# Kernel optimization log

Measured on AMD Instinct MI355X. Metric: run time of the kernel, lower is better.

The kernel has to match this reference:

```python
import jax, jax.numpy as jnp
import numpy as np

N_LEVELS = 16
N_FEATS = 2
LOG2_T = 19
TABLE_SIZE = 1 << LOG2_T
BASE_RES = 16
FINEST_RES = 512
DIM = 3
N_POINTS = 2_000_000
PRIMES = jnp.array([1, 2654435761, 805459861], dtype=jnp.uint32)


def _hash_encode(x01, tables, resolutions):
    """Multi-resolution hash grid encoding with trilinear interpolation.
    x01: [N, D] in [0, 1]; tables: [L, T, F]; resolutions: [L] float.
    Returns [N, L*F]."""
    N, D = x01.shape
    T = tables.shape[1]
    # all 2^D corner offsets of the enclosing voxel, shape [2^D, D]
    offsets = jnp.array([[(i >> d) & 1 for d in range(D)] for i in range(1 << D)],
                        dtype=jnp.float32)

    def per_level(table, res):
        pos = x01 * res                      # [N, D]
        p0 = jnp.floor(pos)
        w = pos - p0                         # fractional part, [N, D]
        corners = p0[None, :, :] + offsets[:, None, :]      # [2^D, N, D]
        ci = corners.astype(jnp.uint32)
        hp = ci * PRIMES[None, None, :D]                    # uint32 wraps mod 2^32
        h = hp[..., 0]
        for d in range(1, D):
            h = h ^ hp[..., d]
        idx = (h & jnp.uint32(T - 1)).astype(jnp.int32)     # [2^D, N]
        feats = table[idx]                                  # gather, [2^D, N, F]
        # trilinear weights: prod_d (w_d if corner bit set else 1-w_d)
        wc = jnp.prod(jnp.where(offsets[:, None, :] > 0, w[None], 1.0 - w[None]),
                      axis=-1)                              # [2^D, N]
        return jnp.sum(wc[..., None] * feats, axis=0)       # [N, F]

    f = jax.vmap(per_level)(tables, resolutions)            # [L, N, F]
    return jnp.transpose(f, (1, 0, 2)).reshape(N, -1)       # [N, L*F]


def setup_inputs() -> dict:
    key = jax.random.key(0)
    ks = jax.random.split(key, 8)
    x = jax.random.uniform(ks[0], (N_POINTS, DIM), jnp.float32, -1.0, 1.0)
    tables = jax.random.uniform(ks[1], (N_LEVELS, TABLE_SIZE, N_FEATS),
                                jnp.float32, -1e-4, 1e-4)
    b = np.exp((np.log(FINEST_RES) - np.log(BASE_RES)) / (N_LEVELS - 1))
    resolutions = jnp.asarray(np.floor(BASE_RES * b ** np.arange(N_LEVELS)),
                              dtype=jnp.float32)
    in_dim = N_LEVELS * N_FEATS  # 32
    W1 = jax.random.normal(ks[2], (in_dim, 64), jnp.float32) * (1.0 / np.sqrt(in_dim))
    b1 = jnp.zeros((64,), jnp.float32)
    W2 = jax.random.normal(ks[3], (64, 64), jnp.float32) * (1.0 / 8.0)
    b2 = jnp.zeros((64,), jnp.float32)
    W3 = jax.random.normal(ks[4], (64, 1), jnp.float32) * (1.0 / 8.0)
    b3 = jnp.zeros((1,), jnp.float32)
    return {"x": x, "tables": tables, "resolutions": resolutions,
            "W1": W1, "b1": b1, "W2": W2, "b2": b2, "W3": W3, "b3": b3}


def reference(x, tables, resolutions, W1, b1, W2, b2, W3, b3):
    x01 = x / 2.0 + 0.5                       # map [-1,1] -> [0,1]
    a = _hash_encode(x01, tables, resolutions)  # [N, 32]
    h = jax.nn.relu(a @ W1 + b1)
    h = jax.nn.relu(h @ W2 + b2)
    return h @ W3 + b3                        # [N, 1]
```

## Files before the change

kernel.cpp:

```cpp
#include <hip/hip_runtime.h>
#include <hip/hip_bf16.h>
#include <stdint.h>

#define N_LEVELS   16
#define LOG2_T     19
#define TABLE_SIZE (1u << LOG2_T)
#define PRIME_Y    2654435761u
#define PRIME_Z    805459861u

#define NB        32768
#define SORT_B    256

typedef float v4f __attribute__((ext_vector_type(4)));
typedef _Float16 v8h __attribute__((ext_vector_type(8)));

__device__ __forceinline__ uint32_t part1by2(uint32_t v) {
    v &= 0x3FFu;
    v = (v | (v << 16)) & 0x030000FFu;
    v = (v | (v <<  8)) & 0x0300F00Fu;
    v = (v | (v <<  4)) & 0x030C30C3u;
    v = (v | (v <<  2)) & 0x09249249u;
    return v;
}
__device__ __forceinline__ uint32_t morton_key(float xr, float yr, float zr) {
    int vx = (int)((xr * 0.5f + 0.5f) * 32.0f);
    int vy = (int)((yr * 0.5f + 0.5f) * 32.0f);
    int vz = (int)((zr * 0.5f + 0.5f) * 32.0f);
    vx = vx < 0 ? 0 : (vx > 31 ? 31 : vx);
    vy = vy < 0 ? 0 : (vy > 31 ? 31 : vy);
    vz = vz < 0 ? 0 : (vz > 31 ? 31 : vz);
    return part1by2((uint32_t)vx) | (part1by2((uint32_t)vy) << 1)
         | (part1by2((uint32_t)vz) << 2);
}

__global__ __launch_bounds__(256)
void hist_kernel(const float* __restrict__ x, uint32_t* __restrict__ g_hist,
                 int n, int chunk)
{
    __shared__ uint32_t pack[NB / 2];
    const int b = blockIdx.x, t = threadIdx.x;
    for (int w = t; w < NB / 2; w += 256) pack[w] = 0;
    __syncthreads();
    const int beg = b * chunk;
    const int end = (beg + chunk < n) ? (beg + chunk) : n;
    for (int i = beg + t; i < end; i += 256) {
        const uint32_t key = morton_key(x[3*i], x[3*i+1], x[3*i+2]);
        atomicAdd(&pack[key >> 1], 1u << ((key & 1u) << 4));
    }
    __syncthreads();
    uint32_t* __restrict__ dst = g_hist + (size_t)b * NB;
    for (int w = t; w < NB / 2; w += 256) {
        const uint32_t p = pack[w];
        dst[2*w]     = p & 0xFFFFu;
        dst[2*w + 1] = p >> 16;
    }
}

__global__ __launch_bounds__(256)
void scan_cols_kernel(const uint32_t* __restrict__ g_hist,
                      uint32_t* __restrict__ g_part,
                      uint32_t* __restrict__ totals)
{
    const int key = blockIdx.x * 256 + threadIdx.x;
    uint32_t run = 0;
    #pragma unroll 8
    for (int b = 0; b < SORT_B; ++b) {
        const size_t idx = (size_t)b * NB + key;
        const uint32_t v = g_hist[idx];
        g_part[idx] = run;
        run += v;
    }
    totals[key] = run;
}

__global__ void scan_block_kernel(const uint32_t* __restrict__ counts,
                                  uint32_t* __restrict__ prefix,
                                  uint32_t* __restrict__ blocksum) {
    __shared__ uint32_t s[256];
    const int t = threadIdx.x;
    const int i = blockIdx.x * 256 + t;
    const uint32_t v = counts[i];
    s[t] = v; __syncthreads();
    #pragma unroll
    for (int d = 1; d < 256; d <<= 1) {
        const uint32_t u = (t >= d) ? s[t - d] : 0;
        __syncthreads();
        s[t] += u;
        __syncthreads();
    }
    prefix[i] = s[t] - v;
    if (t == 255) blocksum[blockIdx.x] = s[255];
}

__global__ void scan_top_kernel(const uint32_t* __restrict__ blocksum,
                                uint32_t* __restrict__ blockbase, int nb) {
    __shared__ uint32_t s[1024];
    const int t = threadIdx.x;
    const uint32_t v = (t < nb) ? blocksum[t] : 0;
    s[t] = v; __syncthreads();
    #pragma unroll
    for (int d = 1; d < 1024; d <<= 1) {
        const uint32_t u = (t >= d) ? s[t - d] : 0;
        __syncthreads();
        s[t] += u;
        __syncthreads();
    }
    if (t < nb) blockbase[t] = s[t] - v;
}

__global__ void addback_kernel(const uint32_t* __restrict__ prefix,
                               const uint32_t* __restrict__ blockbase,
                               uint32_t* __restrict__ base) {
    const int i = blockIdx.x * 256 + threadIdx.x;
    base[i] = prefix[i] + blockbase[i >> 8];
}

__global__ __launch_bounds__(256)
void scatter_kernel(const float* __restrict__ x,
                    const uint32_t* __restrict__ base,
                    const uint32_t* __restrict__ g_part,
                    float* __restrict__ xs,
                    int* __restrict__ rank_inv,
                    int n, int chunk)
{
    __shared__ uint32_t pack[NB / 2];
    const int b = blockIdx.x, t = threadIdx.x;
    for (int w = t; w < NB / 2; w += 256) pack[w] = 0;
    __syncthreads();
    const uint32_t* __restrict__ part = g_part + (size_t)b * NB;
    const int beg = b * chunk;
    const int end = (beg + chunk < n) ? (beg + chunk) : n;
    for (int i = beg + t; i < end; i += 256) {
        const float a = x[3*i], c = x[3*i+1], d = x[3*i+2];
        const uint32_t key = morton_key(a, c, d);
        const uint32_t sh = (key & 1u) << 4;
        uint32_t r = atomicAdd(&pack[key >> 1], 1u << sh);
        r = (r >> sh) & 0xFFFFu;
        const uint32_t pos = base[key] + part[key] + r;
        xs[pos]         = a;
        xs[n + pos]     = c;
        xs[2*n + pos]   = d;
        rank_inv[i]     = (int)pos;
    }
}

__global__ __launch_bounds__(256, 8)
void encode_kernel(const float* __restrict__ xs,
                   const float* __restrict__ tables,
                   const float* __restrict__ resolutions,
                   _Float16* __restrict__ a_ws,
                   int n)
{
    const int l = blockIdx.y;
    int p = blockIdx.x * blockDim.x + threadIdx.x;
    if (p >= n) p = n - 1;

    const float x0 = xs[p]       * 0.5f + 0.5f;
    const float x1 = xs[n + p]   * 0.5f + 0.5f;
    const float x2 = xs[2*n + p] * 0.5f + 0.5f;

    const float res = resolutions[l];
    const float px = x0 * res, py = x1 * res, pz = x2 * res;
    const float fx = floorf(px), fy = floorf(py), fz = floorf(pz);
    const float wx = px - fx, wy = py - fy, wz = pz - fz;
    const uint32_t cx = (uint32_t)fx;
    const uint32_t cy = (uint32_t)fy;
    const uint32_t cz = (uint32_t)fz;

    const uint32_t hy0 = cy * PRIME_Y, hy1 = hy0 + PRIME_Y;
    const uint32_t hz0 = cz * PRIME_Z, hz1 = hz0 + PRIME_Z;

    const float wx0 = 1.0f - wx, wy0 = 1.0f - wy, wz0 = 1.0f - wz;

    const float* __restrict__ tab = tables + (size_t)l * (size_t)TABLE_SIZE * 2u;

    const uint32_t hyz[4] = { hy0 ^ hz0, hy1 ^ hz0, hy0 ^ hz1, hy1 ^ hz1 };

    float2 cva[4], cvb[4];

    if ((cx & 1u) == 0u) {
        #pragma unroll
        for (int q = 0; q < 4; ++q) {
            const uint32_t idx_a = (cx ^ hyz[q]) & (TABLE_SIZE - 1u);
            const uint32_t base  = idx_a & ~1u;
            const float4 f4 = *(const float4*)(tab + 2u * base);
            const bool hi = (idx_a & 1u) != 0u;
            cva[q] = hi ? make_float2(f4.z, f4.w) : make_float2(f4.x, f4.y);
            cvb[q] = hi ? make_float2(f4.x, f4.y) : make_float2(f4.z, f4.w);
        }
    } else {
        const uint32_t hx0 = cx, hx1 = cx + 1u;
        #pragma unroll
        for (int q = 0; q < 4; ++q) {
            const uint32_t idx_a = (hx0 ^ hyz[q]) & (TABLE_SIZE - 1u);
            const uint32_t idx_b = (hx1 ^ hyz[q]) & (TABLE_SIZE - 1u);
            cva[q] = *(const float2*)(tab + 2u * idx_a);
            cvb[q] = *(const float2*)(tab + 2u * idx_b);
        }
    }

    float f0 = 0.0f, f1 = 0.0f;
    #pragma unroll
    for (int q = 0; q < 4; ++q) {
        const float yf = (q & 1) ? wy : wy0;
        const float zf = (q & 2) ? wz : wz0;
        const float wgt_a = (wx0 * yf) * zf;
        const float wgt_b = (wx  * yf) * zf;
        f0 = fmaf(wgt_a, cva[q].x, f0);
        f1 = fmaf(wgt_a, cva[q].y, f1);
        f0 = fmaf(wgt_b, cvb[q].x, f0);
        f1 = fmaf(wgt_b, cvb[q].y, f1);
    }

    a_ws[(size_t)(2 * l + 0) * n + p] = (_Float16)(f0 * 256.0f);
    a_ws[(size_t)(2 * l + 1) * n + p] = (_Float16)(f1 * 256.0f);
}

__global__ __launch_bounds__(256, 2)
void mlp_mfma_kernel(const _Float16* __restrict__ a_ws,
                     const float* __restrict__ W1,
                     const float* __restrict__ b1,
                     const float* __restrict__ W2,
                     const float* __restrict__ b2,
                     const float* __restrict__ W3,
                     const float* __restrict__ b3,
                     float* __restrict__ outs,
                     int n)
{
    __shared__ float lds[4 * 64 * 16];

    const int lane    = threadIdx.x & 63;
    const int wave_id = threadIdx.x >> 6;
    const int m       = lane & 15;
    const int q       = lane >> 4;
    float* __restrict__ myl = &lds[wave_id * 1024];

    const float b3s = b3[0];

    v8h a1[4];
    #pragma unroll
    for (int t = 0; t < 4; ++t)
        #pragma unroll
        for (int j = 0; j < 8; ++j)
            a1[t][j] = (_Float16)W1[(8 * q + j) * 64 + 16 * t + m];

    v8h a2[2][4];
    #pragma unroll
    for (int c = 0; c < 2; ++c)
        #pragma unroll
        for (int t = 0; t < 4; ++t)
            #pragma unroll
            for (int j = 0; j < 8; ++j)
                a2[c][t][j] = (_Float16)W2[(32 * c + 8 * q + j) * 64 + 16 * t + m];

    float bias1v[16], bias2v[16], w3v[16];
    #pragma unroll
    for (int t = 0; t < 4; ++t)
        #pragma unroll
        for (int r = 0; r < 4; ++r) {
            const int ch = 16 * t + 4 * q + r;
            bias1v[4 * t + r] = 256.0f * b1[ch];
            bias2v[4 * t + r] = 256.0f * b2[ch];
            w3v[4 * t + r]    = W3[ch];
        }

    const int nt = (n + 15) >> 4;
    const int stride = gridDim.x * 4;
    const int gw = blockIdx.x * 4 + wave_id;
    if (gw >= nt) return;

    v8h bh;
    {
        const int p0 = gw * 16;
        const int pr = (p0 + m < n) ? (p0 + m) : (n - 1);
        #pragma unroll
        for (int j = 0; j < 8; ++j)
            bh[j] = a_ws[(size_t)(8 * q + j) * n + pr];
    }

    for (int tile = gw; tile < nt; tile += stride) {
        const int p0 = tile * 16;

        v8h bhn = bh;
        const int nx = tile + stride;
        if (nx < nt) {
            const int p0n = nx * 16;
            const int prn = (p0n + m < n) ? (p0n + m) : (n - 1);
            #pragma unroll
            for (int j = 0; j < 8; ++j)
                bhn[j] = a_ws[(size_t)(8 * q + j) * n + prn];
        }

        v4f acc1[4];
        #pragma unroll
        for (int t = 0; t < 4; ++t) {
            #pragma unroll
            for (int r = 0; r < 4; ++r) acc1[t][r] = bias1v[4 * t + r];
            acc1[t] = __builtin_amdgcn_mfma_f32_16x16x32_f16(a1[t], bh, acc1[t], 0, 0, 0);
        }

        #pragma unroll
        for (int t = 0; t < 4; ++t)
            #pragma unroll
            for (int r = 0; r < 4; ++r)
                myl[(16 * t + 4 * q + r) * 16 + m] = fmaxf(acc1[t][r], 0.0f);
        __threadfence_block();

        v8h b2h[2];
        #pragma unroll
        for (int c = 0; c < 2; ++c)
            #pragma unroll
            for (int j = 0; j < 8; ++j)
                b2h[c][j] = (_Float16)myl[(32 * c + 8 * q + j) * 16 + m];

        v4f acc2[4];
        #pragma unroll
        for (int t = 0; t < 4; ++t) {
            #pragma unroll
            for (int r = 0; r < 4; ++r) acc2[t][r] = bias2v[4 * t + r];
            acc2[t] = __builtin_amdgcn_mfma_f32_16x16x32_f16(a2[0][t], b2h[0], acc2[t], 0, 0, 0);
            acc2[t] = __builtin_amdgcn_mfma_f32_16x16x32_f16(a2[1][t], b2h[1], acc2[t], 0, 0, 0);
        }

        float partial = 0.0f;
        #pragma unroll
        for (int t = 0; t < 4; ++t)
            #pragma unroll
            for (int r = 0; r < 4; ++r)
                partial = fmaf(fmaxf(acc2[t][r], 0.0f), w3v[4 * t + r], partial);

        partial += __shfl_xor(partial, 16);
        partial += __shfl_xor(partial, 32);

        if (q == 0 && p0 + m < n)
            outs[p0 + m] = partial * (1.0f / 256.0f) + b3s;

        bh = bhn;
    }
}

__global__ void unscatter_kernel(const float* __restrict__ outs,
                                 const int* __restrict__ rank_inv,
                                 float* __restrict__ out, int n) {
    const int i = blockIdx.x * blockDim.x + threadIdx.x;
    if (i < n) out[i] = outs[rank_inv[i]];
}

__global__ __launch_bounds__(256, 4)
void hashgrid_mlp_fused(const float* __restrict__ x,
                        const float* __restrict__ tables,
                        const float* __restrict__ resolutions,
                        const float* __restrict__ W1,
                        const float* __restrict__ b1,
                        const float* __restrict__ W2,
                        const float* __restrict__ b2,
                        const float* __restrict__ W3,
                        const float* __restrict__ b3,
                        float* __restrict__ out,
                        int n)
{
    const int i  = blockIdx.x * blockDim.x + threadIdx.x;
    const int ip = (i < n) ? i : (n - 1);

    const float x0 = x[3 * ip + 0] * 0.5f + 0.5f;
    const float x1 = x[3 * ip + 1] * 0.5f + 0.5f;
    const float x2 = x[3 * ip + 2] * 0.5f + 0.5f;

    float h1[64];
    #pragma unroll
    for (int j = 0; j < 64; ++j) h1[j] = b1[j];

    #pragma unroll
    for (int l = 0; l < N_LEVELS; ++l) {
        const float res = resolutions[l];
        const float px = x0 * res, py = x1 * res, pz = x2 * res;
        const float fx = floorf(px), fy = floorf(py), fz = floorf(pz);
        const float wx = px - fx, wy = py - fy, wz = pz - fz;
        const uint32_t cx = (uint32_t)fx;
        const uint32_t cy = (uint32_t)fy;
        const uint32_t cz = (uint32_t)fz;
        const uint32_t hx0 = cx,           hx1 = cx + 1u;
        const uint32_t hy0 = cy * PRIME_Y, hy1 = hy0 + PRIME_Y;
        const uint32_t hz0 = cz * PRIME_Z, hz1 = hz0 + PRIME_Z;
        const float wx0 = 1.0f - wx, wy0 = 1.0f - wy, wz0 = 1.0f - wz;
        const float* __restrict__ tab = tables + (size_t)l * (size_t)TABLE_SIZE * 2u;

        float f0 = 0.0f, f1 = 0.0f;
        #pragma unroll
        for (int c = 0; c < 8; ++c) {
            const uint32_t h = ((c & 1) ? hx1 : hx0) ^
                               ((c & 2) ? hy1 : hy0) ^
                               ((c & 4) ? hz1 : hz0);
            const uint32_t idx = h & (TABLE_SIZE - 1u);
            const float2 fv = *(const float2*)(tab + 2u * idx);
            const float wgt = ((c & 1) ? wx : wx0) *
                              ((c & 2) ? wy : wy0) *
                              ((c & 4) ? wz : wz0);
            f0 = fmaf(wgt, fv.x, f0);
            f1 = fmaf(wgt, fv.y, f1);
        }
        const float* __restrict__ w1a = W1 + (2 * l + 0) * 64;
        const float* __restrict__ w1b = W1 + (2 * l + 1) * 64;
        #pragma unroll
        for (int j = 0; j < 64; ++j)
            h1[j] = fmaf(f1, w1b[j], fmaf(f0, w1a[j], h1[j]));
    }

    #pragma unroll
    for (int j = 0; j < 64; ++j) h1[j] = fmaxf(h1[j], 0.0f);

    float accum = b3[0];
    #pragma unroll
    for (int half = 0; half < 2; ++half) {
        float h2[32];
        #pragma unroll
        for (int j = 0; j < 32; ++j) h2[j] = b2[half * 32 + j];
        #pragma unroll
        for (int k = 0; k < 64; ++k) {
            const float hk = h1[k];
            const float* __restrict__ w2row = W2 + k * 64 + half * 32;
            #pragma unroll
            for (int j = 0; j < 32; ++j)
                h2[j] = fmaf(hk, w2row[j], h2[j]);
        }
        #pragma unroll
        for (int j = 0; j < 32; ++j)
            accum = fmaf(fmaxf(h2[j], 0.0f), W3[half * 32 + j], accum);
    }
    out[ip] = accum;
}

extern "C" void kernel_launch(void* const* d_in, const int* in_sizes, int n_in,
                              void* d_out, int out_size, void* d_ws, size_t ws_size,
                              hipStream_t stream) {
    const float* x           = (const float*)d_in[0];
    const float* tables      = (const float*)d_in[1];
    const float* resolutions = (const float*)d_in[2];
    const float* W1          = (const float*)d_in[3];
    const float* b1          = (const float*)d_in[4];
    const float* W2          = (const float*)d_in[5];
    const float* b2          = (const float*)d_in[6];
    const float* W3          = (const float*)d_in[7];
    const float* b3          = (const float*)d_in[8];
    float* out               = (float*)d_out;

    const int n = out_size;
    const int block = 256;
    const int grid_pts = (n + block - 1) / block;
    const int chunk = (n + SORT_B - 1) / SORT_B;

    size_t off = 0;
    #define CARVE(bytes) (off = (off + 255) & ~(size_t)255, off += (bytes), off - (bytes))
    const size_t aws_off   = CARVE((size_t)32 * n * sizeof(_Float16));
    const size_t xs_off    = CARVE((size_t)3 * n * sizeof(float));
    const size_t rank_off  = CARVE((size_t)n * sizeof(int));
    const size_t outs_off  = CARVE((size_t)n * sizeof(float));
    const size_t tot_off   = CARVE((size_t)NB * sizeof(uint32_t));
    const size_t pref_off  = CARVE((size_t)NB * sizeof(uint32_t));
    const size_t base_off  = CARVE((size_t)NB * sizeof(uint32_t));
    const size_t bsum_off  = CARVE(1024 * sizeof(uint32_t));
    const size_t bbase_off = CARVE(1024 * sizeof(uint32_t));
    const size_t total_ws  = off;
    #undef CARVE

    if (ws_size >= total_ws) {
        char* ws = (char*)d_ws;
        _Float16* a_ws   = (_Float16*)(ws + aws_off);
        uint32_t* g_hist = (uint32_t*)(ws + aws_off);
        uint32_t* g_part = (uint32_t*)(ws + aws_off + (size_t)SORT_B * NB * 4);
        float*    xs     = (float*)(ws + xs_off);
        int*      rank   = (int*)(ws + rank_off);
        float*    outs   = (float*)(ws + outs_off);
        uint32_t* totals = (uint32_t*)(ws + tot_off);
        uint32_t* pref   = (uint32_t*)(ws + pref_off);
        uint32_t* base   = (uint32_t*)(ws + base_off);
        uint32_t* bsum   = (uint32_t*)(ws + bsum_off);
        uint32_t* bbase  = (uint32_t*)(ws + bbase_off);

        hist_kernel<<<SORT_B, block, 0, stream>>>(x, g_hist, n, chunk);
        scan_cols_kernel<<<NB / 256, block, 0, stream>>>(g_hist, g_part, totals);
        scan_block_kernel<<<NB / 256, block, 0, stream>>>(totals, pref, bsum);
        scan_top_kernel<<<1, 1024, 0, stream>>>(bsum, bbase, NB / 256);
        addback_kernel<<<NB / 256, block, 0, stream>>>(pref, bbase, base);
        scatter_kernel<<<SORT_B, block, 0, stream>>>(x, base, g_part, xs, rank, n, chunk);

        dim3 grid_enc(grid_pts, N_LEVELS);
        encode_kernel<<<grid_enc, block, 0, stream>>>(xs, tables, resolutions, a_ws, n);
        mlp_mfma_kernel<<<1024, block, 0, stream>>>(a_ws, W1, b1, W2, b2, W3, b3, outs, n);
        unscatter_kernel<<<grid_pts, block, 0, stream>>>(outs, rank, out, n);
    } else {
        hashgrid_mlp_fused<<<grid_pts, block, 0, stream>>>(
            x, tables, resolutions, W1, b1, W2, b2, W3, b3, out, n);
    }
}
```

Measured before the change: 671.0 us.

## Pack sorted coords as float4, pair features per level, fold unscatter into MLP

The scatter kernel now writes sorted coordinates as one float4 per point and records the inverse permutation (sorted position to original index). The encoder reads a single float4 and writes both features of a level as one packed 32-bit word with a nontemporal store. The MLP kernel reads those packed words with nontemporal loads and writes results straight to the original order through perm. This removes the separate unscatter kernel and its intermediate buffer, and cuts the number of memory transactions. The cost is an extra padding float per point and scattered final writes.

```diff
diff --git a/kernel.cpp b/kernel.cpp
--- a/kernel.cpp
+++ b/kernel.cpp
@@ -119,8 +119,8 @@
 void scatter_kernel(const float* __restrict__ x,
                     const uint32_t* __restrict__ base,
                     const uint32_t* __restrict__ g_part,
-                    float* __restrict__ xs,
-                    int* __restrict__ rank_inv,
+                    float4* __restrict__ xs4,
+                    int* __restrict__ perm,
                     int n, int chunk)
 {
     __shared__ uint32_t pack[NB / 2];
@@ -137,27 +137,26 @@
         uint32_t r = atomicAdd(&pack[key >> 1], 1u << sh);
         r = (r >> sh) & 0xFFFFu;
         const uint32_t pos = base[key] + part[key] + r;
-        xs[pos]         = a;
-        xs[n + pos]     = c;
-        xs[2*n + pos]   = d;
-        rank_inv[i]     = (int)pos;
+        xs4[pos]  = make_float4(a, c, d, 0.0f);
+        perm[pos] = i;
     }
 }
 
 __global__ __launch_bounds__(256, 8)
-void encode_kernel(const float* __restrict__ xs,
+void encode_kernel(const float4* __restrict__ xs4,
                    const float* __restrict__ tables,
                    const float* __restrict__ resolutions,
-                   _Float16* __restrict__ a_ws,
+                   uint32_t* __restrict__ a_ws2,
                    int n)
 {
     const int l = blockIdx.y;
     int p = blockIdx.x * blockDim.x + threadIdx.x;
     if (p >= n) p = n - 1;
 
-    const float x0 = xs[p]       * 0.5f + 0.5f;
-    const float x1 = xs[n + p]   * 0.5f + 0.5f;
-    const float x2 = xs[2*n + p] * 0.5f + 0.5f;
+    const float4 xv = xs4[p];
+    const float x0 = xv.x * 0.5f + 0.5f;
+    const float x1 = xv.y * 0.5f + 0.5f;
+    const float x2 = xv.z * 0.5f + 0.5f;
 
     const float res = resolutions[l];
     const float px = x0 * res, py = x1 * res, pz = x2 * res;
@@ -212,19 +211,22 @@
         f1 = fmaf(wgt_b, cvb[q].y, f1);
     }
 
-    a_ws[(size_t)(2 * l + 0) * n + p] = (_Float16)(f0 * 256.0f);
-    a_ws[(size_t)(2 * l + 1) * n + p] = (_Float16)(f1 * 256.0f);
+    union { _Float16 h[2]; uint32_t u; } pk;
+    pk.h[0] = (_Float16)(f0 * 256.0f);
+    pk.h[1] = (_Float16)(f1 * 256.0f);
+    __builtin_nontemporal_store(pk.u, a_ws2 + (size_t)l * n + p);
 }
 
 __global__ __launch_bounds__(256, 2)
-void mlp_mfma_kernel(const _Float16* __restrict__ a_ws,
+void mlp_mfma_kernel(const uint32_t* __restrict__ a_ws2,
                      const float* __restrict__ W1,
                      const float* __restrict__ b1,
                      const float* __restrict__ W2,
                      const float* __restrict__ b2,
                      const float* __restrict__ W3,
                      const float* __restrict__ b3,
-                     float* __restrict__ outs,
+                     const int* __restrict__ perm,
+                     float* __restrict__ out,
                      int n)
 {
     __shared__ float lds[4 * 64 * 16];
@@ -269,13 +271,18 @@
     const int gw = blockIdx.x * 4 + wave_id;
     if (gw >= nt) return;
 
+    union BF { uint32_t w[4]; v8h h; };
+
     v8h bh;
     {
         const int p0 = gw * 16;
         const int pr = (p0 + m < n) ? (p0 + m) : (n - 1);
-        #pragma unroll
-        for (int j = 0; j < 8; ++j)
-            bh[j] = a_ws[(size_t)(8 * q + j) * n + pr];
+        BF ub;
+        #pragma unroll
+        for (int lv = 0; lv < 4; ++lv)
+            ub.w[lv] = __builtin_nontemporal_load(
+                a_ws2 + (size_t)(4 * q + lv) * n + pr);
+        bh = ub.h;
     }
 
     for (int tile = gw; tile < nt; tile += stride) {
@@ -286,9 +293,12 @@
         if (nx < nt) {
             const int p0n = nx * 16;
             const int prn = (p0n + m < n) ? (p0n + m) : (n - 1);
-            #pragma unroll
-            for (int j = 0; j < 8; ++j)
-                bhn[j] = a_ws[(size_t)(8 * q + j) * n + prn];
+            BF ub;
+            #pragma unroll
+            for (int lv = 0; lv < 4; ++lv)
+                ub.w[lv] = __builtin_nontemporal_load(
+                    a_ws2 + (size_t)(4 * q + lv) * n + prn);
+            bhn = ub.h;
         }
 
         v4f acc1[4];
@@ -333,17 +343,10 @@
         partial += __shfl_xor(partial, 32);
 
         if (q == 0 && p0 + m < n)
-            outs[p0 + m] = partial * (1.0f / 256.0f) + b3s;
+            out[perm[p0 + m]] = partial * (1.0f / 256.0f) + b3s;
 
         bh = bhn;
     }
-}
-
-__global__ void unscatter_kernel(const float* __restrict__ outs,
-                                 const int* __restrict__ rank_inv,
-                                 float* __restrict__ out, int n) {
-    const int i = blockIdx.x * blockDim.x + threadIdx.x;
-    if (i < n) out[i] = outs[rank_inv[i]];
 }
 
 __global__ __launch_bounds__(256, 4)
@@ -451,10 +454,9 @@
 
     size_t off = 0;
     #define CARVE(bytes) (off = (off + 255) & ~(size_t)255, off += (bytes), off - (bytes))
-    const size_t aws_off   = CARVE((size_t)32 * n * sizeof(_Float16));
-    const size_t xs_off    = CARVE((size_t)3 * n * sizeof(float));
-    const size_t rank_off  = CARVE((size_t)n * sizeof(int));
-    const size_t outs_off  = CARVE((size_t)n * sizeof(float));
+    const size_t aws_off   = CARVE((size_t)16 * n * sizeof(uint32_t));
+    const size_t xs_off    = CARVE((size_t)n * sizeof(float4));
+    const size_t perm_off  = CARVE((size_t)n * sizeof(int));
     const size_t tot_off   = CARVE((size_t)NB * sizeof(uint32_t));
     const size_t pref_off  = CARVE((size_t)NB * sizeof(uint32_t));
     const size_t base_off  = CARVE((size_t)NB * sizeof(uint32_t));
@@ -465,12 +467,11 @@
 
     if (ws_size >= total_ws) {
         char* ws = (char*)d_ws;
-        _Float16* a_ws   = (_Float16*)(ws + aws_off);
+        uint32_t* a_ws2  = (uint32_t*)(ws + aws_off);
         uint32_t* g_hist = (uint32_t*)(ws + aws_off);
         uint32_t* g_part = (uint32_t*)(ws + aws_off + (size_t)SORT_B * NB * 4);
-        float*    xs     = (float*)(ws + xs_off);
-        int*      rank   = (int*)(ws + rank_off);
-        float*    outs   = (float*)(ws + outs_off);
+        float4*   xs4    = (float4*)(ws + xs_off);
+        int*      perm   = (int*)(ws + perm_off);
         uint32_t* totals = (uint32_t*)(ws + tot_off);
         uint32_t* pref   = (uint32_t*)(ws + pref_off);
         uint32_t* base   = (uint32_t*)(ws + base_off);
@@ -482,12 +483,12 @@
         scan_block_kernel<<<NB / 256, block, 0, stream>>>(totals, pref, bsum);
         scan_top_kernel<<<1, 1024, 0, stream>>>(bsum, bbase, NB / 256);
         addback_kernel<<<NB / 256, block, 0, stream>>>(pref, bbase, base);
-        scatter_kernel<<<SORT_B, block, 0, stream>>>(x, base, g_part, xs, rank, n, chunk);
+        scatter_kernel<<<SORT_B, block, 0, stream>>>(x, base, g_part, xs4, perm, n, chunk);
 
         dim3 grid_enc(grid_pts, N_LEVELS);
-        encode_kernel<<<grid_enc, block, 0, stream>>>(xs, tables, resolutions, a_ws, n);
-        mlp_mfma_kernel<<<1024, block, 0, stream>>>(a_ws, W1, b1, W2, b2, W3, b3, outs, n);
-        unscatter_kernel<<<grid_pts, block, 0, stream>>>(outs, rank, out, n);
+        encode_kernel<<<grid_enc, block, 0, stream>>>(xs4, tables, resolutions, a_ws2, n);
+        mlp_mfma_kernel<<<1024, block, 0, stream>>>(a_ws2, W1, b1, W2, b2, W3, b3,
+                                                    perm, out, n);
     } else {
         hashgrid_mlp_fused<<<grid_pts, block, 0, stream>>>(
             x, tables, resolutions, W1, b1, W2, b2, W3, b3, out, n);
```

After: 646.1 us. 1.04x faster.
